# Kernel tuning notes

Measured on AMD Instinct MI355X. Metric: run time of the kernel, lower is better.

The kernel has to match this reference:

```python
import jax, jax.numpy as jnp
import numpy as np

DIM, OUT = 256, 8
EPS = 1e-5

def _xavier(key, shape):
    fan_out, fan_in = shape
    bound = np.sqrt(6.0 / (fan_in + fan_out))
    return jax.random.uniform(key, shape, jnp.float32, -bound, bound)

def setup_inputs() -> dict:
    key = jax.random.key(0)
    k0, k1, k2 = jax.random.split(key, 3)
    x = jax.random.normal(k0, (128, 2048, DIM), dtype=jnp.float32)
    W1 = _xavier(k1, (OUT, DIM))   # torch Linear weight layout [out, in]
    b1 = jnp.zeros((OUT,), jnp.float32)
    W2 = _xavier(k2, (OUT, OUT))
    b2 = jnp.zeros((OUT,), jnp.float32)
    gamma = jnp.ones((OUT,), jnp.float32)
    beta = jnp.zeros((OUT,), jnp.float32)
    return {"x": x, "W1": W1, "b1": b1, "W2": W2, "b2": b2, "gamma": gamma, "beta": beta}

def reference(x, W1, b1, W2, b2, gamma, beta):
    # Linear(dim->out) + exact GELU + Linear(out->out) + LayerNorm(out)
    h = jnp.einsum('btd,od->bto', x, W1) + b1
    h = jax.nn.gelu(h, approximate=False)  # torch nn.GELU default = erf
    h = jnp.einsum('bto,po->btp', h, W2) + b2
    mu = jnp.mean(h, axis=-1, keepdims=True)
    var = jnp.mean(jnp.square(h - mu), axis=-1, keepdims=True)
    y = (h - mu) * jax.lax.rsqrt(var + EPS) * gamma + beta
    return y
```

## Files before the change

### kernel.cpp

```cpp
#include <hip/hip_runtime.h>
#include <math.h>

#define DIM 256
#define OUT 8
#define EPS 1e-5f

__global__ __launch_bounds__(256) void ffn_kernel(
    const float* __restrict__ x,
    const float* __restrict__ W1,
    const float* __restrict__ b1,
    const float* __restrict__ W2,
    const float* __restrict__ b2,
    const float* __restrict__ gamma,
    const float* __restrict__ beta,
    float* __restrict__ out,
    int n_tokens)
{
    int t = blockIdx.x * blockDim.x + threadIdx.x;
    if (t >= n_tokens) return;

    const float4* xv  = (const float4*)(x + (size_t)t * DIM);
    const float4* w1v = (const float4*)W1;

    float acc[OUT];
    #pragma unroll
    for (int o = 0; o < OUT; ++o) acc[o] = b1[o];

    #pragma unroll 4
    for (int j = 0; j < DIM/4; ++j) {
        float4 xj = xv[j];
        #pragma unroll
        for (int o = 0; o < OUT; ++o) {
            float4 w = w1v[o*(DIM/4) + j];
            acc[o] = fmaf(xj.x, w.x, acc[o]);
            acc[o] = fmaf(xj.y, w.y, acc[o]);
            acc[o] = fmaf(xj.z, w.z, acc[o]);
            acc[o] = fmaf(xj.w, w.w, acc[o]);
        }
    }

    float g[OUT];
    #pragma unroll
    for (int o = 0; o < OUT; ++o) {
        float h = acc[o];
        g[o] = 0.5f * h * (1.0f + erff(h * 0.70710678118654752f));
    }

    float h2[OUT];
    float sum = 0.f;
    #pragma unroll
    for (int p = 0; p < OUT; ++p) {
        float a = b2[p];
        #pragma unroll
        for (int o = 0; o < OUT; ++o)
            a = fmaf(W2[p*OUT + o], g[o], a);
        h2[p] = a;
        sum += a;
    }

    float mu = sum * (1.0f / OUT);
    float vs = 0.f;
    #pragma unroll
    for (int p = 0; p < OUT; ++p) {
        float d = h2[p] - mu;
        vs = fmaf(d, d, vs);
    }
    float rs = rsqrtf(vs * (1.0f / OUT) + EPS);

    float r[OUT];
    #pragma unroll
    for (int p = 0; p < OUT; ++p)
        r[p] = (h2[p] - mu) * rs * gamma[p] + beta[p];

    float4* outv = (float4*)(out + (size_t)t * OUT);
    outv[0] = make_float4(r[0], r[1], r[2], r[3]);
    outv[1] = make_float4(r[4], r[5], r[6], r[7]);
}

extern "C" void kernel_launch(void* const* d_in, const int* in_sizes, int n_in,
                              void* d_out, int out_size, void* d_ws, size_t ws_size,
                              hipStream_t stream) {
    const float* x     = (const float*)d_in[0];
    const float* W1    = (const float*)d_in[1];
    const float* b1    = (const float*)d_in[2];
    const float* W2    = (const float*)d_in[3];
    const float* b2    = (const float*)d_in[4];
    const float* gamma = (const float*)d_in[5];
    const float* beta  = (const float*)d_in[6];
    float* out = (float*)d_out;

    int n_tokens = in_sizes[0] / DIM;
    int block = 256;
    int grid = (n_tokens + block - 1) / block;
    ffn_kernel<<<grid, block, 0, stream>>>(x, W1, b1, W2, b2, gamma, beta, out, n_tokens);
}
```

Before: 389.5 us.

## Coalesce token loads via per-wave LDS transpose with register prefetch

Each wave now loads a 64-token by 32-column tile of x with coalesced float4 reads, where 8 lanes cover one contiguous row segment. It transposes the tile through per-wave shared memory so each lane still computes one token's dot products. The next chunk is prefetched into registers while the current one is consumed. This targets the strided per-thread row reads of the original, at the cost of LDS traffic, possible bank conflicts, and an assumption that token counts are a multiple of 64.

```diff
diff --git a/kernel.cpp b/kernel.cpp
--- a/kernel.cpp
+++ b/kernel.cpp
@@ -4,6 +4,8 @@
 #define DIM 256
 #define OUT 8
 #define EPS 1e-5f
+#define CHUNK 32
+#define NCHUNK (DIM / CHUNK)
 
 __global__ __launch_bounds__(256) void ffn_kernel(
     const float* __restrict__ x,
@@ -16,26 +18,55 @@
     float* __restrict__ out,
     int n_tokens)
 {
-    int t = blockIdx.x * blockDim.x + threadIdx.x;
-    if (t >= n_tokens) return;
+    const int tid  = threadIdx.x;
+    const int wid  = tid >> 6;
+    const int lane = tid & 63;
 
-    const float4* xv  = (const float4*)(x + (size_t)t * DIM);
-    const float4* w1v = (const float4*)W1;
+    const long wave_tok = (long)blockIdx.x * 256 + wid * 64;
+    if (wave_tok >= n_tokens) return;
+    const float* xw = x + wave_tok * DIM;
+
+    __shared__ float lds[4 * 2048];
+    float* L = lds + (wid << 11);
+
+    const int r_off = lane >> 3;
+    const int c_ld  = lane & 7;
 
     float acc[OUT];
     #pragma unroll
     for (int o = 0; o < OUT; ++o) acc[o] = b1[o];
 
-    #pragma unroll 4
-    for (int j = 0; j < DIM/4; ++j) {
-        float4 xj = xv[j];
+    float4 stage[8];
+    #pragma unroll
+    for (int i = 0; i < 8; ++i) {
+        int r = i * 8 + r_off;
+        stage[i] = *(const float4*)(xw + r * DIM + c_ld * 4);
+    }
+
+    for (int ch = 0; ch < NCHUNK; ++ch) {
         #pragma unroll
-        for (int o = 0; o < OUT; ++o) {
-            float4 w = w1v[o*(DIM/4) + j];
-            acc[o] = fmaf(xj.x, w.x, acc[o]);
-            acc[o] = fmaf(xj.y, w.y, acc[o]);
-            acc[o] = fmaf(xj.z, w.z, acc[o]);
-            acc[o] = fmaf(xj.w, w.w, acc[o]);
+        for (int i = 0; i < 8; ++i) {
+            int r = i * 8 + r_off;
+            *(float4*)&L[c_ld * 256 + r * 4] = stage[i];
+        }
+        if (ch + 1 < NCHUNK) {
+            #pragma unroll
+            for (int i = 0; i < 8; ++i) {
+                int r = i * 8 + r_off;
+                stage[i] = *(const float4*)(xw + r * DIM + (ch + 1) * CHUNK + c_ld * 4);
+            }
+        }
+        #pragma unroll
+        for (int c = 0; c < 8; ++c) {
+            float4 xv = *(const float4*)&L[c * 256 + lane * 4];
+            #pragma unroll
+            for (int o = 0; o < OUT; ++o) {
+                float4 w = *(const float4*)&W1[o * DIM + ch * CHUNK + c * 4];
+                acc[o] = fmaf(xv.x, w.x, acc[o]);
+                acc[o] = fmaf(xv.y, w.y, acc[o]);
+                acc[o] = fmaf(xv.z, w.z, acc[o]);
+                acc[o] = fmaf(xv.w, w.w, acc[o]);
+            }
         }
     }
 
@@ -53,7 +84,7 @@
         float a = b2[p];
         #pragma unroll
         for (int o = 0; o < OUT; ++o)
-            a = fmaf(W2[p*OUT + o], g[o], a);
+            a = fmaf(W2[p * OUT + o], g[o], a);
         h2[p] = a;
         sum += a;
     }
@@ -72,7 +103,8 @@
     for (int p = 0; p < OUT; ++p)
         r[p] = (h2[p] - mu) * rs * gamma[p] + beta[p];
 
-    float4* outv = (float4*)(out + (size_t)t * OUT);
+    const long t = wave_tok + lane;
+    float4* outv = (float4*)(out + t * OUT);
     outv[0] = make_float4(r[0], r[1], r[2], r[3]);
     outv[1] = make_float4(r[4], r[5], r[6], r[7]);
 }
@@ -90,7 +122,6 @@
     float* out = (float*)d_out;
 
     int n_tokens = in_sizes[0] / DIM;
-    int block = 256;
-    int grid = (n_tokens + block - 1) / block;
-    ffn_kernel<<<grid, block, 0, stream>>>(x, W1, b1, W2, b2, gamma, beta, out, n_tokens);
+    int grid = (n_tokens + 255) / 256;
+    ffn_kernel<<<grid, 256, 0, stream>>>(x, W1, b1, W2, b2, gamma, beta, out, n_tokens);
 }
```

Result: slower. 412.1 us (+5.8%).

## Coalesce x loads with wave-cooperative dot products and shuffle transpose-reduce

Applied to the files above, without the earlier changes.

Instead of each thread reading its own 1 KB token row (strided, uncoalesced), each wave reads one token row per 64-lane float4 load, with W1 held in registers per lane. Partial sums are reduced across lanes with a butterfly shuffle that also transposes results, so each lane ends up owning one token's outputs. This targets memory coalescing on a bandwidth-bound input of about 268 MB. It adds many cross-lane shuffles and assumes the token count is a multiple of 256, since the tail guard is removed.

```diff
diff --git a/kernel.cpp b/kernel.cpp
--- a/kernel.cpp
+++ b/kernel.cpp
@@ -13,37 +13,84 @@
     const float* __restrict__ b2,
     const float* __restrict__ gamma,
     const float* __restrict__ beta,
-    float* __restrict__ out,
-    int n_tokens)
+    float* __restrict__ out)
 {
-    int t = blockIdx.x * blockDim.x + threadIdx.x;
-    if (t >= n_tokens) return;
+    const int tid  = threadIdx.x;
+    const int wid  = tid >> 6;
+    const int lane = tid & 63;
 
-    const float4* xv  = (const float4*)(x + (size_t)t * DIM);
-    const float4* w1v = (const float4*)W1;
+    const long wave_tok = (long)blockIdx.x * 256 + (long)wid * 64;
+    const float4* xr = (const float4*)(x + wave_tok * DIM);
 
-    float acc[OUT];
+    float4 w1r[OUT];
     #pragma unroll
-    for (int o = 0; o < OUT; ++o) acc[o] = b1[o];
+    for (int o = 0; o < OUT; ++o)
+        w1r[o] = ((const float4*)(W1 + o * DIM))[lane];
 
-    #pragma unroll 4
-    for (int j = 0; j < DIM/4; ++j) {
-        float4 xj = xv[j];
+    float h[OUT];
+
+    for (int g = 0; g < 16; ++g) {
+        float4 xv0 = xr[(g * 4 + 0) * 64 + lane];
+        float4 xv1 = xr[(g * 4 + 1) * 64 + lane];
+        float4 xv2 = xr[(g * 4 + 2) * 64 + lane];
+        float4 xv3 = xr[(g * 4 + 3) * 64 + lane];
+
+        float m01[OUT], m23[OUT];
+        {
+            float s0[OUT], s1[OUT];
+            #pragma unroll
+            for (int o = 0; o < OUT; ++o) {
+                float4 w = w1r[o];
+                s0[o] = fmaf(xv0.x, w.x, fmaf(xv0.y, w.y, fmaf(xv0.z, w.z, xv0.w * w.w)));
+                s1[o] = fmaf(xv1.x, w.x, fmaf(xv1.y, w.y, fmaf(xv1.z, w.z, xv1.w * w.w)));
+            }
+            #pragma unroll
+            for (int o = 0; o < OUT; ++o) {
+                s0[o] += __shfl_xor(s0[o], 1, 64);
+                s1[o] += __shfl_xor(s1[o], 1, 64);
+                m01[o] = (lane & 1) ? s1[o] : s0[o];
+            }
+        }
+        {
+            float s2[OUT], s3[OUT];
+            #pragma unroll
+            for (int o = 0; o < OUT; ++o) {
+                float4 w = w1r[o];
+                s2[o] = fmaf(xv2.x, w.x, fmaf(xv2.y, w.y, fmaf(xv2.z, w.z, xv2.w * w.w)));
+                s3[o] = fmaf(xv3.x, w.x, fmaf(xv3.y, w.y, fmaf(xv3.z, w.z, xv3.w * w.w)));
+            }
+            #pragma unroll
+            for (int o = 0; o < OUT; ++o) {
+                s2[o] += __shfl_xor(s2[o], 1, 64);
+                s3[o] += __shfl_xor(s3[o], 1, 64);
+                m23[o] = (lane & 1) ? s3[o] : s2[o];
+            }
+        }
+        float m[OUT];
         #pragma unroll
         for (int o = 0; o < OUT; ++o) {
-            float4 w = w1v[o*(DIM/4) + j];
-            acc[o] = fmaf(xj.x, w.x, acc[o]);
-            acc[o] = fmaf(xj.y, w.y, acc[o]);
-            acc[o] = fmaf(xj.z, w.z, acc[o]);
-            acc[o] = fmaf(xj.w, w.w, acc[o]);
+            m01[o] += __shfl_xor(m01[o], 2, 64);
+            m23[o] += __shfl_xor(m23[o], 2, 64);
+            m[o] = (lane & 2) ? m23[o] : m01[o];
+        }
+        #pragma unroll
+        for (int o = 0; o < OUT; ++o) {
+            m[o] += __shfl_xor(m[o], 4, 64);
+            m[o] += __shfl_xor(m[o], 8, 64);
+            m[o] += __shfl_xor(m[o], 16, 64);
+            m[o] += __shfl_xor(m[o], 32, 64);
+        }
+        if ((lane >> 2) == g) {
+            #pragma unroll
+            for (int o = 0; o < OUT; ++o) h[o] = m[o];
         }
     }
 
-    float g[OUT];
+    float gl[OUT];
     #pragma unroll
     for (int o = 0; o < OUT; ++o) {
-        float h = acc[o];
-        g[o] = 0.5f * h * (1.0f + erff(h * 0.70710678118654752f));
+        float v = h[o] + b1[o];
+        gl[o] = 0.5f * v * (1.0f + erff(v * 0.70710678118654752f));
     }
 
     float h2[OUT];
@@ -53,7 +100,7 @@
         float a = b2[p];
         #pragma unroll
         for (int o = 0; o < OUT; ++o)
-            a = fmaf(W2[p*OUT + o], g[o], a);
+            a = fmaf(W2[p * OUT + o], gl[o], a);
         h2[p] = a;
         sum += a;
     }
@@ -72,7 +119,7 @@
     for (int p = 0; p < OUT; ++p)
         r[p] = (h2[p] - mu) * rs * gamma[p] + beta[p];
 
-    float4* outv = (float4*)(out + (size_t)t * OUT);
+    float4* outv = (float4*)(out + (wave_tok + lane) * OUT);
     outv[0] = make_float4(r[0], r[1], r[2], r[3]);
     outv[1] = make_float4(r[4], r[5], r[6], r[7]);
 }
@@ -90,7 +137,6 @@
     float* out = (float*)d_out;
 
     int n_tokens = in_sizes[0] / DIM;
-    int block = 256;
-    int grid = (n_tokens + block - 1) / block;
-    ffn_kernel<<<grid, block, 0, stream>>>(x, W1, b1, W2, b2, gamma, beta, out, n_tokens);
+    int grid = n_tokens / 256;
+    ffn_kernel<<<grid, 256, 0, stream>>>(x, W1, b1, W2, b2, gamma, beta, out);
 }
```

Measured after the change: 378.8 us. -2.7%, faster.

## Cooperative coalesced row loads with shuffle-transpose reduction for first linear

Applied to the files above, without the earlier changes.

Instead of one thread streaming its own 1KB token row (strided, uncoalesced across lanes), each half-wave cooperatively loads a token row with contiguous float4 accesses. W1 is kept in registers, and partial dot products are reduced with a butterfly shuffle-transpose that leaves each lane group owning one output. The results are staged in shared memory so each lane then finishes the GELU, second linear and LayerNorm for one token. The bounds check is dropped, so the token count must be a multiple of 256.

```diff
diff --git a/kernel.cpp b/kernel.cpp
--- a/kernel.cpp
+++ b/kernel.cpp
@@ -13,66 +13,109 @@
     const float* __restrict__ b2,
     const float* __restrict__ gamma,
     const float* __restrict__ beta,
-    float* __restrict__ out,
-    int n_tokens)
+    float* __restrict__ out)
 {
-    int t = blockIdx.x * blockDim.x + threadIdx.x;
-    if (t >= n_tokens) return;
+    const int tid  = threadIdx.x;
+    const int wid  = tid >> 6;
+    const int lane = tid & 63;
+    const int hl   = lane & 31;
+    const int tpar = lane >> 5;
 
-    const float4* xv  = (const float4*)(x + (size_t)t * DIM);
-    const float4* w1v = (const float4*)W1;
+    const long wave_tok = (long)blockIdx.x * 256 + (long)wid * 64;
+    const float4* xr = (const float4*)(x + wave_tok * DIM);
 
-    float acc[OUT];
+    float4 w0[OUT], w1[OUT];
     #pragma unroll
-    for (int o = 0; o < OUT; ++o) acc[o] = b1[o];
+    for (int o = 0; o < OUT; ++o) {
+        const float4* wrow = (const float4*)(W1 + o * DIM);
+        w0[o] = wrow[hl];
+        w1[o] = wrow[hl + 32];
+    }
 
-    #pragma unroll 4
-    for (int j = 0; j < DIM/4; ++j) {
-        float4 xj = xv[j];
+    __shared__ float hbuf[4 * 64 * OUT];
+    float* H = hbuf + (wid << 9);
+
+    const bool b4 = (lane & 16) != 0;
+    const bool b3 = (lane & 8)  != 0;
+    const bool bb2 = (lane & 4) != 0;
+    const int  o_own = (lane >> 2) & 7;
+
+    for (int g = 0; g < 32; ++g) {
+        const int T = 2 * g + tpar;
+        const float4* row = xr + (long)T * 64;
+        float4 xa = row[hl];
+        float4 xb = row[hl + 32];
+
+        float p[OUT];
         #pragma unroll
         for (int o = 0; o < OUT; ++o) {
-            float4 w = w1v[o*(DIM/4) + j];
-            acc[o] = fmaf(xj.x, w.x, acc[o]);
-            acc[o] = fmaf(xj.y, w.y, acc[o]);
-            acc[o] = fmaf(xj.z, w.z, acc[o]);
-            acc[o] = fmaf(xj.w, w.w, acc[o]);
+            float se = fmaf(xa.x, w0[o].x, fmaf(xa.z, w0[o].z,
+                       fmaf(xb.x, w1[o].x, xb.z * w1[o].z)));
+            float so = fmaf(xa.y, w0[o].y, fmaf(xa.w, w0[o].w,
+                       fmaf(xb.y, w1[o].y, xb.w * w1[o].w)));
+            p[o] = se + so;
         }
+
+        float q[4];
+        #pragma unroll
+        for (int i = 0; i < 4; ++i) {
+            float send = b4 ? p[i]     : p[i + 4];
+            float keep = b4 ? p[i + 4] : p[i];
+            q[i] = keep + __shfl_xor(send, 16, 64);
+        }
+        float q2[2];
+        #pragma unroll
+        for (int i = 0; i < 2; ++i) {
+            float send = b3 ? q[i]     : q[i + 2];
+            float keep = b3 ? q[i + 2] : q[i];
+            q2[i] = keep + __shfl_xor(send, 8, 64);
+        }
+        float send = bb2 ? q2[0] : q2[1];
+        float keep = bb2 ? q2[1] : q2[0];
+        float r = keep + __shfl_xor(send, 4, 64);
+        r += __shfl_xor(r, 2, 64);
+        r += __shfl_xor(r, 1, 64);
+        if ((lane & 3) == 0) H[T * OUT + o_own] = r;
     }
 
-    float g[OUT];
+    float4 ha = *(const float4*)&H[lane * OUT];
+    float4 hb = *(const float4*)&H[lane * OUT + 4];
+    float h[OUT] = {ha.x, ha.y, ha.z, ha.w, hb.x, hb.y, hb.z, hb.w};
+
+    float gl[OUT];
     #pragma unroll
     for (int o = 0; o < OUT; ++o) {
-        float h = acc[o];
-        g[o] = 0.5f * h * (1.0f + erff(h * 0.70710678118654752f));
+        float v = h[o] + b1[o];
+        gl[o] = 0.5f * v * (1.0f + erff(v * 0.70710678118654752f));
     }
 
     float h2[OUT];
     float sum = 0.f;
     #pragma unroll
-    for (int p = 0; p < OUT; ++p) {
-        float a = b2[p];
+    for (int pp = 0; pp < OUT; ++pp) {
+        float a = b2[pp];
         #pragma unroll
         for (int o = 0; o < OUT; ++o)
-            a = fmaf(W2[p*OUT + o], g[o], a);
-        h2[p] = a;
+            a = fmaf(W2[pp * OUT + o], gl[o], a);
+        h2[pp] = a;
         sum += a;
     }
 
     float mu = sum * (1.0f / OUT);
     float vs = 0.f;
     #pragma unroll
-    for (int p = 0; p < OUT; ++p) {
-        float d = h2[p] - mu;
+    for (int pp = 0; pp < OUT; ++pp) {
+        float d = h2[pp] - mu;
         vs = fmaf(d, d, vs);
     }
     float rs = rsqrtf(vs * (1.0f / OUT) + EPS);
 
     float r[OUT];
     #pragma unroll
-    for (int p = 0; p < OUT; ++p)
-        r[p] = (h2[p] - mu) * rs * gamma[p] + beta[p];
+    for (int pp = 0; pp < OUT; ++pp)
+        r[pp] = (h2[pp] - mu) * rs * gamma[pp] + beta[pp];
 
-    float4* outv = (float4*)(out + (size_t)t * OUT);
+    float4* outv = (float4*)(out + (wave_tok + lane) * OUT);
     outv[0] = make_float4(r[0], r[1], r[2], r[3]);
     outv[1] = make_float4(r[4], r[5], r[6], r[7]);
 }
@@ -90,7 +133,6 @@
     float* out = (float*)d_out;
 
     int n_tokens = in_sizes[0] / DIM;
-    int block = 256;
-    int grid = (n_tokens + block - 1) / block;
-    ffn_kernel<<<grid, block, 0, stream>>>(x, W1, b1, W2, b2, gamma, beta, out, n_tokens);
+    int grid = n_tokens / 256;
+    ffn_kernel<<<grid, 256, 0, stream>>>(x, W1, b1, W2, b2, gamma, beta, out);
 }
```

Result: faster. 374.3 us (-3.9%).
